# Optimization experiments

Measured on AMD Instinct MI355X. Metric: run time of the kernel, lower is better.

Reference implementation:

```python
import jax, jax.numpy as jnp
import numpy as np

EMBED_DIM = 1024
NUM_HEADS = 16
HEAD_DIM = EMBED_DIM // NUM_HEADS


def setup_inputs() -> dict:
    key = jax.random.key(0)
    k1, k2, k3 = jax.random.split(key, 3)
    B, S = 2, 2048
    x = jax.random.normal(k1, (B, S, EMBED_DIM), dtype=jnp.float32)
    # Xavier-uniform-style init for dense kernels
    lim_qkv = float(np.sqrt(6.0 / (EMBED_DIM + 3 * EMBED_DIM)))
    w_qkv = jax.random.uniform(k2, (EMBED_DIM, 3 * EMBED_DIM), jnp.float32, -lim_qkv, lim_qkv)
    b_qkv = jnp.zeros((3 * EMBED_DIM,), jnp.float32)
    lim_out = float(np.sqrt(6.0 / (EMBED_DIM + EMBED_DIM)))
    w_out = jax.random.uniform(k3, (EMBED_DIM, EMBED_DIM), jnp.float32, -lim_out, lim_out)
    b_out = jnp.zeros((EMBED_DIM,), jnp.float32)
    return {"x": x, "w_qkv": w_qkv, "b_qkv": b_qkv, "w_out": w_out, "b_out": b_out}


def reference(x, w_qkv, b_qkv, w_out, b_out):
    B, S, E = x.shape
    qkv = x @ w_qkv + b_qkv                       # [B, S, 3E]
    qkv = qkv.reshape(B, S, NUM_HEADS, 3 * HEAD_DIM)
    qkv = qkv.transpose(0, 2, 1, 3)               # [B, H, S, 3*dh]
    q, k, v = jnp.split(qkv, 3, axis=-1)          # each [B, H, S, dh]
    scale = 1.0 / jnp.sqrt(jnp.asarray(HEAD_DIM, x.dtype))
    logits = jnp.einsum('bhqd,bhkd->bhqk', q, k) * scale  # [B, H, S, S]
    attn = jax.nn.softmax(logits, axis=-1)
    vals = jnp.einsum('bhqk,bhkd->bhqd', attn, v)  # [B, H, S, dh]
    vals = vals.transpose(0, 2, 1, 3).reshape(B, S, E)
    return vals @ w_out + b_out
```

## Files before the change

kernel.cpp:

```cpp
#include <hip/hip_runtime.h>
#include <cstdint>

typedef unsigned short u16;
typedef unsigned int u32;
typedef __attribute__((ext_vector_type(8))) short bf16x8;
typedef __attribute__((ext_vector_type(4))) float f32x4;

#if __has_builtin(__builtin_amdgcn_exp2f)
#define EXP2(x) __builtin_amdgcn_exp2f(x)
#else
#define EXP2(x) exp2f(x)
#endif

__device__ __forceinline__ u16 f2bf(float f) {
  unsigned u = __float_as_uint(f);
  u += 0x7fffu + ((u >> 16) & 1u);
  return (u16)(u >> 16);
}
__device__ __forceinline__ u32 pk_bf16(float lo, float hi) {
#if __has_builtin(__builtin_amdgcn_cvt_pk_bf16_f32)
  auto r = __builtin_amdgcn_cvt_pk_bf16_f32(lo, hi);
  return __builtin_bit_cast(u32, r);
#else
  u32 a = __float_as_uint(lo), b = __float_as_uint(hi);
  a += 0x7fffu + ((a >> 16) & 1u);
  b += 0x7fffu + ((b >> 16) & 1u);
  return (a >> 16) | (b & 0xffff0000u);
#endif
}

__device__ __forceinline__ void async_load16(const void* g, void* l) {
  typedef const __attribute__((address_space(1))) void* gp_t;
  typedef __attribute__((address_space(3))) void* lp_t;
  __builtin_amdgcn_global_load_lds((gp_t)(uintptr_t)g, (lp_t)(uintptr_t)l, 16, 0, 0);
}

__global__ __launch_bounds__(256) void cvt_f32_bf16(
    const float* __restrict__ src, u16* __restrict__ dst)
{
  const size_t i = ((size_t)blockIdx.x * 256 + threadIdx.x) * 8;
  const float4 a = *(const float4*)(src + i);
  const float4 b = *(const float4*)(src + i + 4);
  union { u16 u[8]; bf16x8 v; } p;
  p.u[0] = f2bf(a.x); p.u[1] = f2bf(a.y); p.u[2] = f2bf(a.z); p.u[3] = f2bf(a.w);
  p.u[4] = f2bf(b.x); p.u[5] = f2bf(b.y); p.u[6] = f2bf(b.z); p.u[7] = f2bf(b.w);
  *(bf16x8*)(dst + i) = p.v;
}

__global__ __launch_bounds__(256) void transpose_cvt(
    const float* __restrict__ src, u16* __restrict__ dst, int rows, int cols)
{
  __shared__ u16 tile[64][65];
  const int t = threadIdx.x;
  const int r = t >> 2, c0 = (t & 3) * 16;
  const int tr = blockIdx.y * 64, tc = blockIdx.x * 64;
  const float* sp = src + (size_t)(tr + r) * cols + tc + c0;
#pragma unroll
  for (int i = 0; i < 16; i += 4) {
    const float4 v = *(const float4*)(sp + i);
    tile[r][c0 + i + 0] = f2bf(v.x);
    tile[r][c0 + i + 1] = f2bf(v.y);
    tile[r][c0 + i + 2] = f2bf(v.z);
    tile[r][c0 + i + 3] = f2bf(v.w);
  }
  __syncthreads();
  u16* dp = dst + (size_t)(tc + r) * rows + tr + c0;
#pragma unroll
  for (int i = 0; i < 16; ++i) dp[i] = tile[c0 + i][r];
}

template <int MODE>
__global__ __launch_bounds__(256) void gemm_bt(
    const u16* __restrict__ A, const u16* __restrict__ Bt, const float* __restrict__ bias,
    u16* __restrict__ Qp, u16* __restrict__ Kp, u16* __restrict__ Vtp,
    float* __restrict__ Outp, int Kd)
{
  __shared__ __align__(16) u16 As[128 * 32];
  __shared__ __align__(16) u16 Bs[128 * 32];
  const int t = threadIdx.x;
  const int lane = t & 63, wave = t >> 6;
  const int quad = lane >> 4, m16 = lane & 15;
  const int mb = blockIdx.y * 128, nb = blockIdx.x * 128;
  const int wr = (wave & 1) * 64, wc = (wave >> 1) * 64;

  const int srow = t >> 2;
  const int scol = (t & 3) * 8;
  const u16* Ag0 = A + (size_t)(mb + srow) * Kd + scol;
  const u16* Ag1 = Ag0 + (size_t)64 * Kd;
  const u16* Bg0 = Bt + (size_t)(nb + srow) * Kd + scol;
  const u16* Bg1 = Bg0 + (size_t)64 * Kd;
  u16* AsD = As + t * 8;
  u16* BsD = Bs + t * 8;

  f32x4 acc[4][4] = {};

  for (int k0 = 0; k0 < Kd; k0 += 32) {
    __syncthreads();
    async_load16(Ag0 + k0, AsD);
    async_load16(Ag1 + k0, AsD + 2048);
    async_load16(Bg0 + k0, BsD);
    async_load16(Bg1 + k0, BsD + 2048);
    __syncthreads();
    bf16x8 af[4], bfr[4];
#pragma unroll
    for (int i = 0; i < 4; ++i)
      af[i] = *(const bf16x8*)(As + (wr + i * 16 + m16) * 32 + quad * 8);
#pragma unroll
    for (int i = 0; i < 4; ++i)
      bfr[i] = *(const bf16x8*)(Bs + (wc + i * 16 + m16) * 32 + quad * 8);
#pragma unroll
    for (int i = 0; i < 4; ++i)
#pragma unroll
      for (int j = 0; j < 4; ++j)
        acc[i][j] = __builtin_amdgcn_mfma_f32_16x16x32_bf16(af[i], bfr[j], acc[i][j], 0, 0, 0);
  }

#pragma unroll
  for (int j = 0; j < 4; ++j) {
    const int base = nb + wc + j * 16;
    const float bv = bias[base + m16];
    if (MODE == 1) {
#pragma unroll
      for (int i = 0; i < 4; ++i)
#pragma unroll
        for (int r = 0; r < 4; ++r) {
          const int row = mb + wr + i * 16 + quad * 4 + r;
          Outp[(size_t)row * 1024 + base + m16] = acc[i][j][r] + bv;
        }
    } else {
      const int seg = base >> 6;
      const int h = seg / 3;
      const int which = seg - h * 3;
      const int d = (base & 63) + m16;
      const float qs = (which == 0) ? 0.18033688011112042f : 1.0f;
#pragma unroll
      for (int i = 0; i < 4; ++i)
#pragma unroll
        for (int r = 0; r < 4; ++r) {
          const int row = mb + wr + i * 16 + quad * 4 + r;
          const int b = row >> 11, sI = row & 2047;
          const u16 v = f2bf((acc[i][j][r] + bv) * qs);
          const size_t bh = (size_t)((b << 4) | h);
          if (which == 0)      Qp[(bh * 2048 + sI) * 64 + d] = v;
          else if (which == 1) Kp[(bh * 2048 + sI) * 64 + d] = v;
          else                 Vtp[(bh * 64 + d) * 2048 + sI] = v;
        }
    }
  }
}

__global__ __launch_bounds__(256) void flash_attn(
    const u16* __restrict__ Q, const u16* __restrict__ K, const u16* __restrict__ Vt,
    u16* __restrict__ O)
{
  const int S = 2048;
  __shared__ __align__(16) u16 Kl[2][64 * 64];
  __shared__ __align__(16) u16 Vl[2][64 * 64];
  __shared__ __align__(16) u32 Pl[4][16 * 32];
  const int t = threadIdx.x;
  const int lane = t & 63, w = t >> 6;
  const int quad = lane >> 4, m16 = lane & 15;

  const int f = blockIdx.x;
  const int wi = f >> 3;
  const int bh = (f & 7) + 8 * (wi & 3);
  const int q0 = (wi >> 2) * 64;

  const u16* Qb = Q + (size_t)bh * S * 64;
  const u16* Kb = K + (size_t)bh * S * 64;
  const u16* Vb = Vt + (size_t)bh * 64 * S;

  bf16x8 qf[2];
#pragma unroll
  for (int ks = 0; ks < 2; ++ks)
    qf[ks] = *(const bf16x8*)(Qb + (size_t)(q0 + w * 16 + m16) * 64 + ks * 32 + quad * 8);

  const u16* Kg[2]; const u16* Vg[2]; int soff[2];
#pragma unroll
  for (int l = 0; l < 2; ++l) {
    const int idx = l * 256 + t;
    const int row = idx >> 3, slot = idx & 7;
    const int sg = slot ^ (row & 7);
    Kg[l] = Kb + row * 64 + sg * 8;
    Vg[l] = Vb + (size_t)row * S + sg * 8;
    soff[l] = idx * 8;
  }

  f32x4 ot[4] = {};
  f32x4 lr4 = {0.f, 0.f, 0.f, 0.f};
  u32* const Pw = &Pl[w][0];

#pragma unroll
  for (int l = 0; l < 2; ++l) async_load16(Kg[l], &Kl[0][soff[l]]);
#pragma unroll
  for (int l = 0; l < 2; ++l) async_load16(Vg[l], &Vl[0][soff[l]]);
  __syncthreads();

  int buf = 0;
  for (int kv0 = 0; kv0 < S; kv0 += 64, buf ^= 1) {
    if (kv0 + 64 < S) {
      const int nb = buf ^ 1;
#pragma unroll
      for (int l = 0; l < 2; ++l) async_load16(Kg[l] + (kv0 + 64) * 64, &Kl[nb][soff[l]]);
#pragma unroll
      for (int l = 0; l < 2; ++l) async_load16(Vg[l] + (kv0 + 64), &Vl[nb][soff[l]]);
    }
    const u16* Klc = Kl[buf];
    const u16* Vlc = Vl[buf];

    f32x4 st[4] = {};
#pragma unroll
    for (int nt = 0; nt < 4; ++nt) {
      const int j = nt * 16 + m16;
      const u16* rowp = Klc + j * 64;
      const bf16x8 kb0 = *(const bf16x8*)(rowp + ((quad ^ (j & 7)) * 8));
      const bf16x8 kb1 = *(const bf16x8*)(rowp + (((4 + quad) ^ (j & 7)) * 8));
      st[nt] = __builtin_amdgcn_mfma_f32_16x16x32_bf16(kb0, qf[0], st[nt], 0, 0, 0);
      st[nt] = __builtin_amdgcn_mfma_f32_16x16x32_bf16(kb1, qf[1], st[nt], 0, 0, 0);
    }

#pragma unroll
    for (int nt = 0; nt < 4; ++nt) {
      f32x4 p;
#pragma unroll
      for (int r = 0; r < 4; ++r) p[r] = EXP2(st[nt][r]);
      lr4 += p;
      const u32 lo = pk_bf16(p[0], p[1]);
      const u32 hi = pk_bf16(p[2], p[3]);
      const int gp = (2 * nt + (quad >> 1)) ^ (m16 & 7);
      u32* dst = Pw + m16 * 32 + gp * 4 + (quad & 1) * 2;
      *(uint2*)dst = make_uint2(lo, hi);
    }

#pragma unroll
    for (int ks = 0; ks < 2; ++ks) {
      const int pg = (ks * 4 + quad) ^ (m16 & 7);
      const bf16x8 pb = *(const bf16x8*)(Pw + m16 * 32 + pg * 4);
#pragma unroll
      for (int dt = 0; dt < 4; ++dt) {
        const int d = dt * 16 + m16;
        const bf16x8 va = *(const bf16x8*)(Vlc + d * 64 + (((ks * 4 + quad) ^ (d & 7)) * 8));
        ot[dt] = __builtin_amdgcn_mfma_f32_16x16x32_bf16(va, pb, ot[dt], 0, 0, 0);
      }
    }

    __syncthreads();
  }

  float l = lr4[0] + lr4[1] + lr4[2] + lr4[3];
  l += __shfl_xor(l, 16, 64);
  l += __shfl_xor(l, 32, 64);
  const float inv = 1.0f / l;
  const int b = bh >> 4, h = bh & 15;
  const int q = q0 + w * 16 + m16;
  u16* base = O + ((size_t)b * 2048 + q) * 1024 + h * 64;
#pragma unroll
  for (int dt = 0; dt < 4; ++dt) {
    const u32 lo = pk_bf16(ot[dt][0] * inv, ot[dt][1] * inv);
    const u32 hi = pk_bf16(ot[dt][2] * inv, ot[dt][3] * inv);
    *(uint2*)(base + dt * 16 + quad * 4) = make_uint2(lo, hi);
  }
}

extern "C" void kernel_launch(void* const* d_in, const int* in_sizes, int n_in,
                              void* d_out, int out_size, void* d_ws, size_t ws_size,
                              hipStream_t stream)
{
  const float* x     = (const float*)d_in[0];
  const float* w_qkv = (const float*)d_in[1];
  const float* b_qkv = (const float*)d_in[2];
  const float* w_out = (const float*)d_in[3];
  const float* b_out = (const float*)d_in[4];
  float* out = (float*)d_out;

  u16* ws     = (u16*)d_ws;
  u16* xb     = ws;
  u16* WtQKV  = xb + 4194304;
  u16* WtOut  = WtQKV + 3145728;
  u16* Qm     = WtOut + 1048576;
  u16* Km     = Qm + 4194304;
  u16* Vtm    = Km + 4194304;
  u16* AO     = Vtm + 4194304;

  cvt_f32_bf16<<<2048, 256, 0, stream>>>(x, xb);
  transpose_cvt<<<dim3(48, 16), 256, 0, stream>>>(w_qkv, WtQKV, 1024, 3072);
  transpose_cvt<<<dim3(16, 16), 256, 0, stream>>>(w_out, WtOut, 1024, 1024);
  gemm_bt<0><<<dim3(24, 32), 256, 0, stream>>>(xb, WtQKV, b_qkv, Qm, Km, Vtm, nullptr, 1024);
  flash_attn<<<1024, 256, 0, stream>>>(Qm, Km, Vtm, AO);
  gemm_bt<1><<<dim3(8, 32), 256, 0, stream>>>(AO, WtOut, b_out, nullptr, nullptr, nullptr, out, 1024);
}
```

Measured before the change: 211.7 us.

## Write V row-major then transpose separately; use 64-row tiles for output GEMM

```diff
diff --git a/kernel.cpp b/kernel.cpp
--- a/kernel.cpp
+++ b/kernel.cpp
@@ -69,11 +69,35 @@
   for (int i = 0; i < 16; ++i) dp[i] = tile[c0 + i][r];
 }
 
-template <int MODE>
-__global__ __launch_bounds__(256) void gemm_bt(
+__global__ __launch_bounds__(256) void transpose_v(
+    const u16* __restrict__ src, u16* __restrict__ dst)
+{
+  __shared__ u16 tile[64][72];
+  const int t = threadIdx.x;
+  const int r = t >> 2, c0 = (t & 3) * 16;
+  const int bh = blockIdx.y, s0 = blockIdx.x * 64;
+  const u16* sp = src + ((size_t)bh * 2048 + s0 + r) * 64 + c0;
+  union { u16 u[8]; bf16x8 v; } a, b;
+  a.v = *(const bf16x8*)sp;
+  b.v = *(const bf16x8*)(sp + 8);
+#pragma unroll
+  for (int i = 0; i < 8; ++i) tile[r][c0 + i] = a.u[i];
+#pragma unroll
+  for (int i = 0; i < 8; ++i) tile[r][c0 + 8 + i] = b.u[i];
+  __syncthreads();
+  union { u16 u[8]; bf16x8 v; } x, y;
+#pragma unroll
+  for (int i = 0; i < 8; ++i) x.u[i] = tile[c0 + i][r];
+#pragma unroll
+  for (int i = 0; i < 8; ++i) y.u[i] = tile[c0 + 8 + i][r];
+  u16* dp = dst + ((size_t)bh * 64 + r) * 2048 + s0 + c0;
+  *(bf16x8*)dp = x.v;
+  *(bf16x8*)(dp + 8) = y.v;
+}
+
+__global__ __launch_bounds__(256) void gemm_qkv(
     const u16* __restrict__ A, const u16* __restrict__ Bt, const float* __restrict__ bias,
-    u16* __restrict__ Qp, u16* __restrict__ Kp, u16* __restrict__ Vtp,
-    float* __restrict__ Outp, int Kd)
+    u16* __restrict__ Qp, u16* __restrict__ Kp, u16* __restrict__ Vp, int Kd)
 {
   __shared__ __align__(16) u16 As[128 * 32];
   __shared__ __align__(16) u16 Bs[128 * 32];
@@ -119,33 +143,80 @@
   for (int j = 0; j < 4; ++j) {
     const int base = nb + wc + j * 16;
     const float bv = bias[base + m16];
-    if (MODE == 1) {
-#pragma unroll
-      for (int i = 0; i < 4; ++i)
-#pragma unroll
-        for (int r = 0; r < 4; ++r) {
-          const int row = mb + wr + i * 16 + quad * 4 + r;
-          Outp[(size_t)row * 1024 + base + m16] = acc[i][j][r] + bv;
-        }
-    } else {
-      const int seg = base >> 6;
-      const int h = seg / 3;
-      const int which = seg - h * 3;
-      const int d = (base & 63) + m16;
-      const float qs = (which == 0) ? 0.18033688011112042f : 1.0f;
-#pragma unroll
-      for (int i = 0; i < 4; ++i)
-#pragma unroll
-        for (int r = 0; r < 4; ++r) {
-          const int row = mb + wr + i * 16 + quad * 4 + r;
-          const int b = row >> 11, sI = row & 2047;
-          const u16 v = f2bf((acc[i][j][r] + bv) * qs);
-          const size_t bh = (size_t)((b << 4) | h);
-          if (which == 0)      Qp[(bh * 2048 + sI) * 64 + d] = v;
-          else if (which == 1) Kp[(bh * 2048 + sI) * 64 + d] = v;
-          else                 Vtp[(bh * 64 + d) * 2048 + sI] = v;
-        }
-    }
+    const int seg = base >> 6;
+    const int h = seg / 3;
+    const int which = seg - h * 3;
+    const int d = (base & 63) + m16;
+    const float qs = (which == 0) ? 0.18033688011112042f : 1.0f;
+#pragma unroll
+    for (int i = 0; i < 4; ++i)
+#pragma unroll
+      for (int r = 0; r < 4; ++r) {
+        const int row = mb + wr + i * 16 + quad * 4 + r;
+        const int b = row >> 11, sI = row & 2047;
+        const u16 v = f2bf((acc[i][j][r] + bv) * qs);
+        const size_t idx = (((size_t)((b << 4) | h)) * 2048 + sI) * 64 + d;
+        if (which == 0)      Qp[idx] = v;
+        else if (which == 1) Kp[idx] = v;
+        else                 Vp[idx] = v;
+      }
+  }
+}
+
+__global__ __launch_bounds__(256) void gemm_out(
+    const u16* __restrict__ A, const u16* __restrict__ Bt, const float* __restrict__ bias,
+    float* __restrict__ Outp)
+{
+  const int Kd = 1024;
+  __shared__ __align__(16) u16 As[64 * 32];
+  __shared__ __align__(16) u16 Bs[128 * 32];
+  const int t = threadIdx.x;
+  const int lane = t & 63, wave = t >> 6;
+  const int quad = lane >> 4, m16 = lane & 15;
+  const int mb = blockIdx.y * 64, nb = blockIdx.x * 128;
+  const int wr = (wave & 1) * 32, wc = (wave >> 1) * 64;
+
+  const int srow = t >> 2;
+  const int scol = (t & 3) * 8;
+  const u16* Ag0 = A + (size_t)(mb + srow) * Kd + scol;
+  const u16* Bg0 = Bt + (size_t)(nb + srow) * Kd + scol;
+  const u16* Bg1 = Bg0 + (size_t)64 * Kd;
+  u16* AsD = As + t * 8;
+  u16* BsD = Bs + t * 8;
+
+  f32x4 acc[2][4] = {};
+
+  for (int k0 = 0; k0 < Kd; k0 += 32) {
+    __syncthreads();
+    async_load16(Ag0 + k0, AsD);
+    async_load16(Bg0 + k0, BsD);
+    async_load16(Bg1 + k0, BsD + 2048);
+    __syncthreads();
+    bf16x8 af[2], bfr[4];
+#pragma unroll
+    for (int i = 0; i < 2; ++i)
+      af[i] = *(const bf16x8*)(As + (wr + i * 16 + m16) * 32 + quad * 8);
+#pragma unroll
+    for (int j = 0; j < 4; ++j)
+      bfr[j] = *(const bf16x8*)(Bs + (wc + j * 16 + m16) * 32 + quad * 8);
+#pragma unroll
+    for (int i = 0; i < 2; ++i)
+#pragma unroll
+      for (int j = 0; j < 4; ++j)
+        acc[i][j] = __builtin_amdgcn_mfma_f32_16x16x32_bf16(af[i], bfr[j], acc[i][j], 0, 0, 0);
+  }
+
+#pragma unroll
+  for (int j = 0; j < 4; ++j) {
+    const int col = nb + wc + j * 16 + m16;
+    const float bv = bias[col];
+#pragma unroll
+    for (int i = 0; i < 2; ++i)
+#pragma unroll
+      for (int r = 0; r < 4; ++r) {
+        const int row = mb + wr + i * 16 + quad * 4 + r;
+        Outp[(size_t)row * 1024 + col] = acc[i][j][r] + bv;
+      }
   }
 }
 
@@ -281,11 +352,13 @@
   u16* Km     = Qm + 4194304;
   u16* Vtm    = Km + 4194304;
   u16* AO     = Vtm + 4194304;
+  u16* Vm     = AO;
 
   cvt_f32_bf16<<<2048, 256, 0, stream>>>(x, xb);
   transpose_cvt<<<dim3(48, 16), 256, 0, stream>>>(w_qkv, WtQKV, 1024, 3072);
   transpose_cvt<<<dim3(16, 16), 256, 0, stream>>>(w_out, WtOut, 1024, 1024);
-  gemm_bt<0><<<dim3(24, 32), 256, 0, stream>>>(xb, WtQKV, b_qkv, Qm, Km, Vtm, nullptr, 1024);
+  gemm_qkv<<<dim3(24, 32), 256, 0, stream>>>(xb, WtQKV, b_qkv, Qm, Km, Vm, 1024);
+  transpose_v<<<dim3(32, 32), 256, 0, stream>>>(Vm, Vtm);
   flash_attn<<<1024, 256, 0, stream>>>(Qm, Km, Vtm, AO);
-  gemm_bt<1><<<dim3(8, 32), 256, 0, stream>>>(AO, WtOut, b_out, nullptr, nullptr, nullptr, out, 1024);
-}
+  gemm_out<<<dim3(8, 64), 256, 0, stream>>>(AO, WtOut, b_out, out);
+}
```

Result: faster. 204.7 us (-3.3%).
